# Kernel tuning notes

Measured on AMD Instinct MI355X. Metric: run time of the kernel, lower is better.

Reference implementation:

```python
import jax, jax.numpy as jnp
import numpy as np

B, S, H, NH = 4, 2048, 1024, 16
HD = H // NH  # head_size = 64


def setup_inputs() -> dict:
    key = jax.random.key(0)
    ks = jax.random.split(key, 12)
    s = 1.0 / np.sqrt(H)
    return {
        "query": jax.random.normal(ks[0], (B, S, H), jnp.float32),
        "key": jax.random.normal(ks[1], (B, S, H), jnp.float32),
        "value": jax.random.normal(ks[2], (B, S, H), jnp.float32),
        "attention_mask": jax.random.randint(ks[3], (B, 1, S, S), 0, 2).astype(jnp.float32),
        "Wq": jax.random.normal(ks[4], (H, H), jnp.float32) * s,
        "bq": jnp.zeros((H,), jnp.float32),
        "Wk": jax.random.normal(ks[5], (H, H), jnp.float32) * s,
        "bk": jnp.zeros((H,), jnp.float32),
        "Wv": jax.random.normal(ks[6], (H, H), jnp.float32) * s,
        "bv": jnp.zeros((H,), jnp.float32),
        "Wo": jax.random.normal(ks[7], (H, H), jnp.float32) * s,
        "bo": jnp.zeros((H,), jnp.float32),
    }


def reference(query, key, value, attention_mask, Wq, bq, Wk, bk, Wv, bv, Wo, bo):
    # Linear projections (weights stored [in, out])
    q = query @ Wq + bq   # [B, S, H]
    k = key @ Wk + bk
    v = value @ Wv + bv
    # split heads -> [B, NH, S, HD]
    def heads(x):
        return x.reshape(B, -1, NH, HD).transpose(0, 2, 1, 3)
    q, k, v = heads(q), heads(k), heads(v)
    scale = 1.0 / np.sqrt(HD)
    scores = jnp.einsum("bhqd,bhkd->bhqk", q, k) * scale  # [B, NH, S, S]
    scores = scores + attention_mask * (-1e9)
    attn = jax.nn.softmax(scores, axis=-1)
    # dropout is identity in eval mode (deterministic reference)
    out = jnp.einsum("bhqk,bhkd->bhqd", attn, v)  # [B, NH, S, HD]
    out = out.transpose(0, 2, 1, 3).reshape(B, -1, H)  # [B, S, H]
    return out @ Wo + bo
```

## Files before the change

### kernel.cpp

```cpp
#include <hip/hip_runtime.h>
#include <hip/hip_bf16.h>
#include <stdint.h>

#define B_ 4
#define S_ 2048
#define H_ 1024
#define NH_ 16
#define HD_ 64

typedef __attribute__((ext_vector_type(8))) short short8;
typedef __attribute__((ext_vector_type(4))) float f32x4;
typedef __attribute__((ext_vector_type(4))) unsigned short ushort4v;

__device__ __forceinline__ unsigned short f2bf(float f) {
  union { float f; unsigned u; } x; x.f = f;
  unsigned r = x.u + 0x7fffu + ((x.u >> 16) & 1u);
  return (unsigned short)(r >> 16);
}

#define ALDS16(g, l) \
  __builtin_amdgcn_global_load_lds((const __attribute__((address_space(1))) void*)(g), \
                                   (__attribute__((address_space(3))) void*)(l), 16, 0, 0)

__global__ __launch_bounds__(256) void cvt_in(
    const float* __restrict__ q, const float* __restrict__ k, const float* __restrict__ v,
    unsigned short* __restrict__ oq, unsigned short* __restrict__ ok2, unsigned short* __restrict__ ov) {
  const int z = blockIdx.z;
  const float* src = z == 0 ? q : (z == 1 ? k : v);
  unsigned short* dst = z == 0 ? oq : (z == 1 ? ok2 : ov);
  const size_t i = ((size_t)blockIdx.x * 256 + threadIdx.x) * 8;
  const f32x4 a = *reinterpret_cast<const f32x4*>(src + i);
  const f32x4 c = *reinterpret_cast<const f32x4*>(src + i + 4);
  short8 o;
#pragma unroll
  for (int j = 0; j < 4; ++j) { o[j] = (short)f2bf(a[j]); o[j + 4] = (short)f2bf(c[j]); }
  *reinterpret_cast<short8*>(dst + i) = o;
}

__global__ __launch_bounds__(256) void packmask(
    const float* __restrict__ mask, unsigned long long* __restrict__ mb) {
  const int w = threadIdx.x >> 6, lane = threadIdx.x & 63;
  const int wbase = (blockIdx.x * 4 + w) * 32;
#pragma unroll 8
  for (int i = 0; i < 32; ++i) {
    const float v = mask[(size_t)(wbase + i) * 64 + lane];
    const unsigned long long bits = __ballot(v == 0.0f);
    if (lane == 0) mb[wbase + i] = bits;
  }
}

__global__ __launch_bounds__(256) void cvt_w(
    const float* __restrict__ Wq, const float* __restrict__ Wk,
    const float* __restrict__ Wv, const float* __restrict__ Wo,
    unsigned short* __restrict__ wt) {
  __shared__ float tile[64][65];
  const int z = blockIdx.z;
  const float* W = z == 0 ? Wq : (z == 1 ? Wk : (z == 2 ? Wv : Wo));
  unsigned short* out = wt + (size_t)z * H_ * H_;
  const int t = threadIdx.x;
  const int r0 = blockIdx.y * 64, c0 = blockIdx.x * 64;
  const int tr = t >> 4, tc = (t & 15) * 4;
#pragma unroll
  for (int rr = 0; rr < 4; ++rr) {
    const int row = rr * 16 + tr;
    const f32x4 val = *reinterpret_cast<const f32x4*>(W + (size_t)(r0 + row) * H_ + c0 + tc);
#pragma unroll
    for (int j = 0; j < 4; ++j) tile[row][tc + j] = val[j];
  }
  __syncthreads();
#pragma unroll
  for (int rr = 0; rr < 4; ++rr) {
    const int c = rr * 16 + tr;
    ushort4v o;
#pragma unroll
    for (int j = 0; j < 4; ++j) o[j] = f2bf(tile[tc + j][c]);
    *reinterpret_cast<ushort4v*>(out + (size_t)(c0 + c) * H_ + r0 + tc) = o;
  }
}

template <int OUTMODE>
__device__ __forceinline__ void gemm_body(
    const unsigned short* __restrict__ X, const unsigned short* __restrict__ Wt,
    const float* __restrict__ bias, float oscale, unsigned short* __restrict__ obf,
    float* __restrict__ of32) {
  __shared__ unsigned short As[128 * 32];
  __shared__ unsigned short Bs[128 * 32];
  const int t = threadIdx.x;
  const int w = t >> 6, l = t & 63;
  const int lr = l & 15, lg = l >> 4;
  const int brow = blockIdx.x * 128, bcol = blockIdx.y * 128;
  const int wr = (w >> 1) * 64, wc = (w & 1) * 64;
  f32x4 acc[4][4] = {};
  const int i0 = t, i1 = t + 256;
  const int ar0 = i0 >> 2, ak0 = (i0 & 3) * 8;
  const int ar1 = i1 >> 2, ak1 = (i1 & 3) * 8;
  for (int kt = 0; kt < 1024; kt += 32) {
    ALDS16(X + (size_t)(brow + ar0) * 1024 + kt + ak0, As + i0 * 8);
    ALDS16(X + (size_t)(brow + ar1) * 1024 + kt + ak1, As + i1 * 8);
    ALDS16(Wt + (size_t)(bcol + ar0) * 1024 + kt + ak0, Bs + i0 * 8);
    ALDS16(Wt + (size_t)(bcol + ar1) * 1024 + kt + ak1, Bs + i1 * 8);
    __syncthreads();
    short8 af[4], bf[4];
#pragma unroll
    for (int m = 0; m < 4; ++m)
      af[m] = *reinterpret_cast<const short8*>(As + (wr + m * 16 + lr) * 32 + lg * 8);
#pragma unroll
    for (int n = 0; n < 4; ++n)
      bf[n] = *reinterpret_cast<const short8*>(Bs + (wc + n * 16 + lr) * 32 + lg * 8);
#pragma unroll
    for (int m = 0; m < 4; ++m)
#pragma unroll
      for (int n = 0; n < 4; ++n)
        acc[m][n] = __builtin_amdgcn_mfma_f32_16x16x32_bf16(af[m], bf[n], acc[m][n], 0, 0, 0);
    __syncthreads();
  }
#pragma unroll
  for (int m = 0; m < 4; ++m) {
#pragma unroll
    for (int n = 0; n < 4; ++n) {
#pragma unroll
      for (int r = 0; r < 4; ++r) {
        const int gr = brow + wr + m * 16 + lg * 4 + r;
        const int gc = bcol + wc + n * 16 + lr;
        const float val = (acc[m][n][r] + bias[gc]) * oscale;
        if (OUTMODE == 0) {
          const int bb = gr >> 11, ss = gr & 2047, hh = gc >> 6, dd = gc & 63;
          obf[(((size_t)(bb * NH_ + hh)) * S_ + ss) * HD_ + dd] = f2bf(val);
        } else {
          of32[(size_t)gr * H_ + gc] = val;
        }
      }
    }
  }
}

#define QSCL 0.1803368801111244f

__global__ __launch_bounds__(256) void gemm_qkv(
    const unsigned short* __restrict__ xq, const unsigned short* __restrict__ xk,
    const unsigned short* __restrict__ xv, const unsigned short* __restrict__ wt,
    const float* __restrict__ bq, const float* __restrict__ bk, const float* __restrict__ bv,
    unsigned short* __restrict__ qh, unsigned short* __restrict__ kh,
    unsigned short* __restrict__ vh) {
  const int z = blockIdx.z;
  const unsigned short* X = z == 0 ? xq : (z == 1 ? xk : xv);
  const unsigned short* W = wt + (size_t)z * H_ * H_;
  const float* bias = z == 0 ? bq : (z == 1 ? bk : bv);
  unsigned short* out = z == 0 ? qh : (z == 1 ? kh : vh);
  const float scl = z == 0 ? QSCL : 1.0f;
  gemm_body<0>(X, W, bias, scl, out, nullptr);
}

__global__ __launch_bounds__(256) void gemm_out(
    const unsigned short* __restrict__ ao, const unsigned short* __restrict__ wt,
    const float* __restrict__ bo, float* __restrict__ out) {
  gemm_body<1>(ao, wt, bo, 1.0f, nullptr, out);
}

__global__ __launch_bounds__(256) void vtrans(
    const unsigned short* __restrict__ vh, unsigned short* __restrict__ vt) {
  __shared__ unsigned short tile[64 * 72];
  const int bh = blockIdx.y;
  const int s0 = blockIdx.x * 64;
  const int t = threadIdx.x;
  const unsigned short* src = vh + (size_t)bh * S_ * HD_ + (size_t)s0 * HD_;
#pragma unroll
  for (int r = 0; r < 2; ++r) {
    const int i = t + r * 256;
    const int row = i >> 3, kc = i & 7;
    const short8 v = *reinterpret_cast<const short8*>(src + row * 64 + kc * 8);
    *reinterpret_cast<short8*>(tile + row * 72 + kc * 8) = v;
  }
  __syncthreads();
  unsigned short* dst = vt + (size_t)bh * HD_ * S_;
#pragma unroll
  for (int r = 0; r < 2; ++r) {
    const int i = t + r * 256;
    const int d = i >> 3, sc = i & 7;
    short8 o;
#pragma unroll
    for (int j = 0; j < 8; ++j) o[j] = (short)tile[(sc * 8 + j) * 72 + d];
    *reinterpret_cast<short8*>(dst + (size_t)d * S_ + s0 + sc * 8) = o;
  }
}

__global__ __launch_bounds__(256, 2) void attn_kernel(
    const unsigned short* __restrict__ qh, const unsigned short* __restrict__ kh,
    const unsigned short* __restrict__ vt, const unsigned long long* __restrict__ mb,
    unsigned short* __restrict__ ao) {
  __shared__ unsigned short Ks[2][64 * 64];
  __shared__ unsigned short Vs[2][64 * 64];
  __shared__ unsigned short Ps[4][16 * 64 * 3];
  const int t = threadIdx.x, w = t >> 6, l = t & 63;
  const int lr = l & 15, lg = l >> 4;
  const int flat = blockIdx.x;
  const int g = flat >> 9;
  const int x = flat & 511;
  const int bh = g * 32 + (x & 7) * 4 + (x >> 7);
  const int qt = (x >> 3) & 15;
  const int b = bh >> 4, h = bh & 15;
  const unsigned short* qptr = qh + (size_t)bh * S_ * HD_;
  const unsigned short* kptr = kh + (size_t)bh * S_ * HD_;
  const unsigned short* vptr = vt + (size_t)bh * HD_ * S_;
  const unsigned long long* mbase = mb + (size_t)b * S_ * (S_ / 64);
  const int qbase = qt * 128 + w * 32;

  short8 qf[2][2];
#pragma unroll
  for (int qs = 0; qs < 2; ++qs) {
    const unsigned short* qp = qptr + (size_t)(qbase + qs * 16 + lr) * HD_ + lg * 8;
    qf[qs][0] = *reinterpret_cast<const short8*>(qp);
    qf[qs][1] = *reinterpret_cast<const short8*>(qp + 32);
  }
  short8 ones;
#pragma unroll
  for (int jj = 0; jj < 8; ++jj) ones[jj] = (short)0x3F80;

  const int si0 = t, si1 = t + 256;
  const int srow0 = si0 >> 3, sk0 = ((si0 & 7) ^ (srow0 & 7)) * 8;
  const int srow1 = si1 >> 3, sk1 = ((si1 & 7) ^ (srow1 & 7)) * 8;
  const unsigned short* ksrc0 = kptr + (size_t)srow0 * HD_ + sk0;
  const unsigned short* ksrc1 = kptr + (size_t)srow1 * HD_ + sk1;
  const unsigned short* vsrc0 = vptr + (size_t)srow0 * S_ + sk0;
  const unsigned short* vsrc1 = vptr + (size_t)srow1 * S_ + sk1;
  size_t moff[2][4];
#pragma unroll
  for (int qs = 0; qs < 2; ++qs)
#pragma unroll
    for (int r = 0; r < 4; ++r)
      moff[qs][r] = (size_t)(qbase + qs * 16 + lg * 4 + r) * (S_ / 64);

  ALDS16(ksrc0, Ks[0] + si0 * 8);
  ALDS16(ksrc1, Ks[0] + si1 * 8);
  ALDS16(vsrc0, Vs[0] + si0 * 8);
  ALDS16(vsrc1, Vs[0] + si1 * 8);
  __syncthreads();

  f32x4 acc_o[2][4] = {};
  f32x4 acc_l[2] = {};
  unsigned short* pw = Ps[w];
  int cur = 0;

  for (int kv = 0; kv < S_; kv += 64) {
    unsigned msel[2][4][4];
#pragma unroll
    for (int qs = 0; qs < 2; ++qs)
#pragma unroll
      for (int r = 0; r < 4; ++r) {
        const unsigned long long mwv = mbase[moff[qs][r] + (kv >> 6)];
        const unsigned long long sh = mwv >> lr;
        const unsigned lo = (unsigned)sh, hi = (unsigned)(sh >> 32);
        msel[qs][r][0] = 0u - (lo & 1u);
        msel[qs][r][1] = 0u - ((lo >> 16) & 1u);
        msel[qs][r][2] = 0u - (hi & 1u);
        msel[qs][r][3] = 0u - ((hi >> 16) & 1u);
      }

    const int nkv = (kv + 64 < S_) ? kv + 64 : 0;
    ALDS16(ksrc0 + (size_t)nkv * HD_, Ks[cur ^ 1] + si0 * 8);
    ALDS16(ksrc1 + (size_t)nkv * HD_, Ks[cur ^ 1] + si1 * 8);
    ALDS16(vsrc0 + nkv, Vs[cur ^ 1] + si0 * 8);
    ALDS16(vsrc1 + nkv, Vs[cur ^ 1] + si1 * 8);

    float p[2][4][4];
#pragma unroll
    for (int n = 0; n < 4; ++n) {
      const int krow = n * 16 + lr;
      const short8 kf0 = *reinterpret_cast<const short8*>(Ks[cur] + krow * 64 + ((0 + lg) ^ (krow & 7)) * 8);
      const short8 kf1 = *reinterpret_cast<const short8*>(Ks[cur] + krow * 64 + ((4 + lg) ^ (krow & 7)) * 8);
#pragma unroll
      for (int qs = 0; qs < 2; ++qs) {
        f32x4 sc = {};
        sc = __builtin_amdgcn_mfma_f32_16x16x32_bf16(qf[qs][0], kf0, sc, 0, 0, 0);
        sc = __builtin_amdgcn_mfma_f32_16x16x32_bf16(qf[qs][1], kf1, sc, 0, 0, 0);
#pragma unroll
        for (int r = 0; r < 4; ++r) {
          union { float f; unsigned u; } cv;
          cv.f = __builtin_amdgcn_exp2f(sc[r]);
          cv.u &= msel[qs][r][n];
          p[qs][n][r] = cv.f;
        }
      }
    }

    short8 pf[2][2];
#pragma unroll
    for (int qs = 0; qs < 2; ++qs) {
#pragma unroll
      for (int r = 0; r < 4; ++r) {
        const int row = lg * 4 + r;
#pragma unroll
        for (int n = 0; n < 4; ++n) {
          union { float f; unsigned u; } cv; cv.f = p[qs][n][r];
          const int col = n * 16 + lr;
          pw[row * 64 + ((col >> 3) ^ (row & 7)) * 8 + (col & 7)] = (unsigned short)(cv.u >> 16);
        }
      }
      pf[qs][0] = *reinterpret_cast<const short8*>(pw + lr * 64 + ((0 + lg) ^ (lr & 7)) * 8);
      pf[qs][1] = *reinterpret_cast<const short8*>(pw + lr * 64 + ((4 + lg) ^ (lr & 7)) * 8);
      acc_l[qs] = __builtin_amdgcn_mfma_f32_16x16x32_bf16(pf[qs][0], ones, acc_l[qs], 0, 0, 0);
      acc_l[qs] = __builtin_amdgcn_mfma_f32_16x16x32_bf16(pf[qs][1], ones, acc_l[qs], 0, 0, 0);
    }

#pragma unroll
    for (int d = 0; d < 4; ++d) {
      const int vrow = d * 16 + lr;
      const short8 vf0 = *reinterpret_cast<const short8*>(Vs[cur] + vrow * 64 + ((0 + lg) ^ (vrow & 7)) * 8);
      const short8 vf1 = *reinterpret_cast<const short8*>(Vs[cur] + vrow * 64 + ((4 + lg) ^ (vrow & 7)) * 8);
#pragma unroll
      for (int qs = 0; qs < 2; ++qs) {
        acc_o[qs][d] = __builtin_amdgcn_mfma_f32_16x16x32_bf16(pf[qs][0], vf0, acc_o[qs][d], 0, 0, 0);
        acc_o[qs][d] = __builtin_amdgcn_mfma_f32_16x16x32_bf16(pf[qs][1], vf1, acc_o[qs][d], 0, 0, 0);
      }
    }
    __syncthreads();
    cur ^= 1;
  }

#pragma unroll
  for (int qs = 0; qs < 2; ++qs)
#pragma unroll
    for (int r = 0; r < 4; ++r) {
      const float inv = __builtin_amdgcn_rcpf(acc_l[qs][r]);
      const int qrow = qbase + qs * 16 + lg * 4 + r;
      unsigned short* orow = ao + ((size_t)b * S_ + qrow) * H_ + h * HD_;
#pragma unroll
      for (int d = 0; d < 4; ++d)
        orow[d * 16 + lr] = f2bf(acc_o[qs][d][r] * inv);
    }
}

extern "C" void kernel_launch(void* const* d_in, const int* in_sizes, int n_in,
                              void* d_out, int out_size, void* d_ws, size_t ws_size,
                              hipStream_t stream) {
  (void)in_sizes; (void)n_in; (void)out_size; (void)ws_size;
  const float* query = (const float*)d_in[0];
  const float* key_  = (const float*)d_in[1];
  const float* value = (const float*)d_in[2];
  const float* mask  = (const float*)d_in[3];
  const float* Wq = (const float*)d_in[4];
  const float* bq = (const float*)d_in[5];
  const float* Wk = (const float*)d_in[6];
  const float* bk = (const float*)d_in[7];
  const float* Wv = (const float*)d_in[8];
  const float* bv = (const float*)d_in[9];
  const float* Wo = (const float*)d_in[10];
  const float* bo = (const float*)d_in[11];
  float* out = (float*)d_out;

  char* ws = (char*)d_ws;
  const size_t MB16 = (size_t)1 << 24;
  unsigned short* XQ = (unsigned short*)(ws + 0 * MB16);
  unsigned short* XK = (unsigned short*)(ws + 1 * MB16);
  unsigned short* XV = (unsigned short*)(ws + 2 * MB16);
  unsigned short* QH = (unsigned short*)(ws + 3 * MB16);
  unsigned short* KH = (unsigned short*)(ws + 4 * MB16);
  unsigned short* VH = (unsigned short*)(ws + 5 * MB16);
  unsigned short* WT = (unsigned short*)(ws + 6 * MB16);
  unsigned long long* MBits = (unsigned long long*)(ws + 6 * MB16 + (size_t)4 * H_ * H_ * 2);
  unsigned short* AO = XQ;
  unsigned short* VT = XK;

  cvt_in<<<dim3(4096, 1, 3), 256, 0, stream>>>(query, key_, value, XQ, XK, XV);
  packmask<<<dim3(2048), 256, 0, stream>>>(mask, MBits);
  cvt_w<<<dim3(16, 16, 4), 256, 0, stream>>>(Wq, Wk, Wv, Wo, WT);
  gemm_qkv<<<dim3(64, 8, 3), 256, 0, stream>>>(XQ, XK, XV, WT, bq, bk, bv, QH, KH, VH);
  vtrans<<<dim3(32, 64), 256, 0, stream>>>(VH, VT);
  attn_kernel<<<dim3(1024), 256, 0, stream>>>(QH, KH, VT, MBits, AO);
  gemm_out<<<dim3(64, 8, 1), 256, 0, stream>>>(AO, WT + 3 * (size_t)H_ * H_, bo, out);
}
```

Measured before the change: 282.3 us.

## Deepen GEMM K-tile to 64 with XOR-swizzled LDS and raise occupancy hints

The projection GEMMs now stage 64-wide K tiles instead of 32, which halves the number of barrier pairs per output tile. Shared memory is laid out with an XOR swizzle so the fragment reads avoid bank conflicts. Launch bounds request 4 blocks per CU, and the attention PV MFMA loop is wrapped in s_setprio to favour that wave. In exchange, each block uses twice as much LDS and the occupancy hint may constrain register allocation.

```diff
diff --git a/kernel.cpp b/kernel.cpp
--- a/kernel.cpp
+++ b/kernel.cpp
@@ -83,35 +83,49 @@
     const unsigned short* __restrict__ X, const unsigned short* __restrict__ Wt,
     const float* __restrict__ bias, float oscale, unsigned short* __restrict__ obf,
     float* __restrict__ of32) {
-  __shared__ unsigned short As[128 * 32];
-  __shared__ unsigned short Bs[128 * 32];
+  __shared__ unsigned short As[128 * 64];
+  __shared__ unsigned short Bs[128 * 64];
   const int t = threadIdx.x;
   const int w = t >> 6, l = t & 63;
   const int lr = l & 15, lg = l >> 4;
   const int brow = blockIdx.x * 128, bcol = blockIdx.y * 128;
   const int wr = (w >> 1) * 64, wc = (w & 1) * 64;
   f32x4 acc[4][4] = {};
-  const int i0 = t, i1 = t + 256;
-  const int ar0 = i0 >> 2, ak0 = (i0 & 3) * 8;
-  const int ar1 = i1 >> 2, ak1 = (i1 & 3) * 8;
-  for (int kt = 0; kt < 1024; kt += 32) {
-    ALDS16(X + (size_t)(brow + ar0) * 1024 + kt + ak0, As + i0 * 8);
-    ALDS16(X + (size_t)(brow + ar1) * 1024 + kt + ak1, As + i1 * 8);
-    ALDS16(Wt + (size_t)(bcol + ar0) * 1024 + kt + ak0, Bs + i0 * 8);
-    ALDS16(Wt + (size_t)(bcol + ar1) * 1024 + kt + ak1, Bs + i1 * 8);
+  const unsigned short* xb = X + (size_t)brow * 1024;
+  const unsigned short* wb = Wt + (size_t)bcol * 1024;
+  int srow[4], skl[4];
+#pragma unroll
+  for (int j = 0; j < 4; ++j) {
+    const int c = t + j * 256;
+    srow[j] = c >> 3;
+    skl[j] = ((c & 7) ^ ((c >> 3) & 7)) * 8;
+  }
+  for (int kt = 0; kt < 1024; kt += 64) {
+#pragma unroll
+    for (int j = 0; j < 4; ++j) {
+      ALDS16(xb + (size_t)srow[j] * 1024 + kt + skl[j], As + (t + j * 256) * 8);
+      ALDS16(wb + (size_t)srow[j] * 1024 + kt + skl[j], Bs + (t + j * 256) * 8);
+    }
     __syncthreads();
-    short8 af[4], bf[4];
-#pragma unroll
-    for (int m = 0; m < 4; ++m)
-      af[m] = *reinterpret_cast<const short8*>(As + (wr + m * 16 + lr) * 32 + lg * 8);
-#pragma unroll
-    for (int n = 0; n < 4; ++n)
-      bf[n] = *reinterpret_cast<const short8*>(Bs + (wc + n * 16 + lr) * 32 + lg * 8);
-#pragma unroll
-    for (int m = 0; m < 4; ++m)
-#pragma unroll
-      for (int n = 0; n < 4; ++n)
-        acc[m][n] = __builtin_amdgcn_mfma_f32_16x16x32_bf16(af[m], bf[n], acc[m][n], 0, 0, 0);
+#pragma unroll
+    for (int kk = 0; kk < 2; ++kk) {
+      short8 af[4], bf[4];
+#pragma unroll
+      for (int m = 0; m < 4; ++m) {
+        const int ra = wr + m * 16 + lr;
+        af[m] = *reinterpret_cast<const short8*>(As + ra * 64 + ((kk * 4 + lg) ^ (ra & 7)) * 8);
+      }
+#pragma unroll
+      for (int n = 0; n < 4; ++n) {
+        const int rb = wc + n * 16 + lr;
+        bf[n] = *reinterpret_cast<const short8*>(Bs + rb * 64 + ((kk * 4 + lg) ^ (rb & 7)) * 8);
+      }
+#pragma unroll
+      for (int m = 0; m < 4; ++m)
+#pragma unroll
+        for (int n = 0; n < 4; ++n)
+          acc[m][n] = __builtin_amdgcn_mfma_f32_16x16x32_bf16(af[m], bf[n], acc[m][n], 0, 0, 0);
+    }
     __syncthreads();
   }
 #pragma unroll
@@ -136,7 +150,7 @@
 
 #define QSCL 0.1803368801111244f
 
-__global__ __launch_bounds__(256) void gemm_qkv(
+__global__ __launch_bounds__(256, 4) void gemm_qkv(
     const unsigned short* __restrict__ xq, const unsigned short* __restrict__ xk,
     const unsigned short* __restrict__ xv, const unsigned short* __restrict__ wt,
     const float* __restrict__ bq, const float* __restrict__ bk, const float* __restrict__ bv,
@@ -151,7 +165,7 @@
   gemm_body<0>(X, W, bias, scl, out, nullptr);
 }
 
-__global__ __launch_bounds__(256) void gemm_out(
+__global__ __launch_bounds__(256, 4) void gemm_out(
     const unsigned short* __restrict__ ao, const unsigned short* __restrict__ wt,
     const float* __restrict__ bo, float* __restrict__ out) {
   gemm_body<1>(ao, wt, bo, 1.0f, nullptr, out);
@@ -302,6 +316,7 @@
       acc_l[qs] = __builtin_amdgcn_mfma_f32_16x16x32_bf16(pf[qs][1], ones, acc_l[qs], 0, 0, 0);
     }
 
+    __builtin_amdgcn_s_setprio(1);
 #pragma unroll
     for (int d = 0; d < 4; ++d) {
       const int vrow = d * 16 + lr;
@@ -313,6 +328,7 @@
         acc_o[qs][d] = __builtin_amdgcn_mfma_f32_16x16x32_bf16(pf[qs][1], vf1, acc_o[qs][d], 0, 0, 0);
       }
     }
+    __builtin_amdgcn_s_setprio(0);
     __syncthreads();
     cur ^= 1;
   }
```

Measured after the change: 266.2 us. -5.7%, faster.
